# Performance work log

Hardware: AMD Instinct MI355X
Metric: run time of the kernel (lower is better)

## Reference

```python
import jax, jax.numpy as jnp
import numpy as np
import math
from jax import lax

B, T, GS = 16, 511, 1
OBS, OUT = 60, 30
D, H, L = 1024, 16, 8
DFF, HID = 4096, 100
S = T + GS
DH = D // H
EPS = 1e-5


def _ln(x, g, b):
    m = jnp.mean(x, axis=-1, keepdims=True)
    v = jnp.mean(jnp.square(x - m), axis=-1, keepdims=True)
    return (x - m) * lax.rsqrt(v + EPS) * g + b


def setup_inputs():
    key = jax.random.key(0)
    ks = iter(jax.random.split(key, 32))
    def n(shape):
        return jax.random.normal(next(ks), shape, dtype=jnp.float32) * 0.02
    return {
        "states": jax.random.normal(next(ks), (B, T, OBS), dtype=jnp.float32),
        "goals": jax.random.normal(next(ks), (B, GS, OBS), dtype=jnp.float32),
        "Wtok": n((OBS, D)), "btok": jnp.zeros((D,), jnp.float32),
        "pos": n((1, S, D)),
        "ln1_g": jnp.ones((L, D), jnp.float32), "ln1_b": jnp.zeros((L, D), jnp.float32),
        "Wq": n((L, D, D)), "bq": jnp.zeros((L, D), jnp.float32),
        "Wk": n((L, D, D)), "bk": jnp.zeros((L, D), jnp.float32),
        "Wv": n((L, D, D)), "bv": jnp.zeros((L, D), jnp.float32),
        "Wp": n((L, D, D)), "bp": jnp.zeros((L, D), jnp.float32),
        "ln2_g": jnp.ones((L, D), jnp.float32), "ln2_b": jnp.zeros((L, D), jnp.float32),
        "Wm1": n((L, D, DFF)), "bm1": jnp.zeros((L, DFF), jnp.float32),
        "Wm2": n((L, DFF, D)), "bm2": jnp.zeros((L, D), jnp.float32),
        "lnf_g": jnp.ones((D,), jnp.float32), "lnf_b": jnp.zeros((D,), jnp.float32),
        "Wh1": n((D, HID)), "bh1": jnp.zeros((HID,), jnp.float32),
        "Wh2": n((HID, OUT)), "bh2": jnp.zeros((OUT,), jnp.float32),
    }


def reference(states, goals, Wtok, btok, pos, ln1_g, ln1_b, Wq, bq, Wk, bk, Wv, bv, Wp, bp,
              ln2_g, ln2_b, Wm1, bm1, Wm2, bm2, lnf_g, lnf_b, Wh1, bh1, Wh2, bh2):
    # token + positional embeddings (dropout is identity in eval mode, pdrop=0)
    goal_x = goals @ Wtok + btok + pos[:, :GS]
    state_x = states @ Wtok + btok + pos[:, GS:S]
    x = jnp.concatenate([goal_x, state_x], axis=1)  # (B, S, D)
    mask = jnp.tril(jnp.ones((S, S), dtype=bool))
    scale = 1.0 / math.sqrt(DH)

    def block(x, p):
        g1, b1, wq, bq_, wk, bk_, wv, bv_, wp, bp_, g2, b2, w1, bm1_, w2, bm2_ = p
        h = _ln(x, g1, b1)
        q = (h @ wq + bq_).reshape(B, S, H, DH).transpose(0, 2, 1, 3)  # (B,H,S,DH)
        k = (h @ wk + bk_).reshape(B, S, H, DH).transpose(0, 2, 1, 3)
        v = (h @ wv + bv_).reshape(B, S, H, DH).transpose(0, 2, 1, 3)
        att = jnp.einsum('bhqd,bhkd->bhqk', q, k) * scale
        att = jnp.where(mask, att, -jnp.inf)
        att = jax.nn.softmax(att, axis=-1)
        y = jnp.einsum('bhqk,bhkd->bhqd', att, v)
        y = y.transpose(0, 2, 1, 3).reshape(B, S, D) @ wp + bp_
        x = x + y
        h = _ln(x, g2, b2)
        x = x + (jax.nn.gelu(h @ w1 + bm1_, approximate=False) @ w2 + bm2_)
        return x, None

    x, _ = lax.scan(block, x, (ln1_g, ln1_b, Wq, bq, Wk, bk, Wv, bv, Wp, bp,
                               ln2_g, ln2_b, Wm1, bm1, Wm2, bm2))
    x = _ln(x, lnf_g, lnf_b)[:, GS:]  # drop goal tokens -> (B, T, D)
    h = jax.nn.silu(x @ Wh1 + bh1)
    return h @ Wh2 + bh2
```

## Files before the change

kernel.cpp:

```cpp
#include <hip/hip_runtime.h>
#include <cstdint>
#include <math.h>

#define NB_B   16
#define NB_T   511
#define NB_S   512
#define NB_OBS 60
#define NB_D   1024
#define NB_H   16
#define NB_L   8
#define NB_DFF 4096
#define NB_HID 100
#define NB_OUT 30
#define NB_M   8192

typedef __attribute__((ext_vector_type(8))) short  short8;
typedef __attribute__((ext_vector_type(4))) short  short4v;
typedef __attribute__((ext_vector_type(4))) float  f32x4;
typedef __attribute__((ext_vector_type(8))) __bf16 bf16x8;

__device__ __forceinline__ short f2bf(float f) {
  union { float f; unsigned u; } a; a.f = f;
  unsigned u = a.u + 0x7fffu + ((a.u >> 16) & 1u);
  return (short)(u >> 16);
}

__device__ __forceinline__ void load_lds16(const void* g, void* l) {
  __builtin_amdgcn_global_load_lds(
      (__attribute__((address_space(1))) unsigned int*)(uintptr_t)g,
      (__attribute__((address_space(3))) unsigned int*)(unsigned)(uintptr_t)l,
      16, 0, 0);
}

__device__ __forceinline__ f32x4 mfma16(short8 a, short8 b, f32x4 c) {
  return __builtin_amdgcn_mfma_f32_16x16x32_bf16(
      __builtin_bit_cast(bf16x8, a), __builtin_bit_cast(bf16x8, b), c, 0, 0, 0);
}

__device__ __forceinline__ float gelu_exact(float v) {
  return 0.5f * v * (1.f + erff(v * 0.70710678118654752f));
}

__global__ __launch_bounds__(256) void tconv_kernel(
    const float* __restrict__ src, short* __restrict__ dst,
    int R, int C, size_t sstride, size_t dstride) {
  __shared__ float t[32][33];
  const float* s0 = src + blockIdx.z * sstride;
  short* d0 = dst + blockIdx.z * dstride;
  const int c0 = blockIdx.x * 32, r0 = blockIdx.y * 32;
  const int tx = threadIdx.x & 31, ty = threadIdx.x >> 5;
#pragma unroll
  for (int i = 0; i < 4; i++)
    t[ty + 8 * i][tx] = s0[(size_t)(r0 + ty + 8 * i) * C + c0 + tx];
  __syncthreads();
#pragma unroll
  for (int i = 0; i < 4; i++)
    d0[(size_t)(c0 + ty + 8 * i) * R + r0 + tx] = f2bf(t[tx][ty + 8 * i]);
}

__global__ __launch_bounds__(256) void whead_prep(
    const float* __restrict__ Wh1, const float* __restrict__ bh1,
    short* __restrict__ Wh1t, float* __restrict__ bh1p) {
  const int idx = blockIdx.x * 256 + threadIdx.x;
  const int n = idx >> 10, k = idx & 1023;
  Wh1t[idx] = (n < NB_HID) ? f2bf(Wh1[k * NB_HID + n]) : (short)0;
  if (idx < 128) bh1p[idx] = (idx < NB_HID) ? bh1[idx] : 0.f;
}

__global__ __launch_bounds__(256) void embed_kernel(
    const float* __restrict__ states, const float* __restrict__ goals,
    const float* __restrict__ Wtok, const float* __restrict__ btok,
    const float* __restrict__ pos, float* __restrict__ x) {
  const int row = blockIdx.x;
  const int b = row >> 9, s = row & (NB_S - 1);
  __shared__ float tok[NB_OBS];
  if (threadIdx.x < NB_OBS)
    tok[threadIdx.x] = (s == 0)
        ? goals[b * NB_OBS + threadIdx.x]
        : states[((size_t)b * NB_T + (s - 1)) * NB_OBS + threadIdx.x];
  __syncthreads();
#pragma unroll
  for (int i = 0; i < 4; i++) {
    const int d = threadIdx.x + i * 256;
    float acc = btok[d] + pos[(size_t)s * NB_D + d];
    for (int o = 0; o < NB_OBS; o++) acc += tok[o] * Wtok[o * NB_D + d];
    x[(size_t)row * NB_D + d] = acc;
  }
}

template <typename OutT>
__global__ __launch_bounds__(256) void ln_kernel(
    const float* __restrict__ xin, const float* __restrict__ gam,
    const float* __restrict__ bet, OutT* __restrict__ outp) {
  const int row = blockIdx.x;
  const int tid = threadIdx.x;
  const float4 v = ((const float4*)(xin + (size_t)row * NB_D))[tid];
  float s = v.x + v.y + v.z + v.w;
  float s2 = v.x * v.x + v.y * v.y + v.z * v.z + v.w * v.w;
#pragma unroll
  for (int o = 32; o; o >>= 1) {
    s += __shfl_down(s, o, 64);
    s2 += __shfl_down(s2, o, 64);
  }
  __shared__ float red[8];
  if ((tid & 63) == 0) { red[tid >> 6] = s; red[4 + (tid >> 6)] = s2; }
  __syncthreads();
  const float S1 = red[0] + red[1] + red[2] + red[3];
  const float S2 = red[4] + red[5] + red[6] + red[7];
  const float mean = S1 * (1.f / NB_D);
  const float var = S2 * (1.f / NB_D) - mean * mean;
  const float rs = rsqrtf(var + 1e-5f);
  const float4 g4 = ((const float4*)gam)[tid];
  const float4 b4 = ((const float4*)bet)[tid];
  const float o0 = (v.x - mean) * rs * g4.x + b4.x;
  const float o1 = (v.y - mean) * rs * g4.y + b4.y;
  const float o2 = (v.z - mean) * rs * g4.z + b4.z;
  const float o3 = (v.w - mean) * rs * g4.w + b4.w;
  if constexpr (sizeof(OutT) == 2) {
    short4v r = {f2bf(o0), f2bf(o1), f2bf(o2), f2bf(o3)};
    *(short4v*)((short*)outp + (size_t)row * NB_D + tid * 4) = r;
  } else {
    ((float4*)((float*)outp + (size_t)row * NB_D))[tid] = make_float4(o0, o1, o2, o3);
  }
}

template <int ACT, bool RESID, typename OutT>
__device__ __forceinline__ void gemm_core(
    const short* __restrict__ A, const short* __restrict__ Bt,
    const float* __restrict__ bias, const float* __restrict__ resid,
    OutT* __restrict__ C, int N, int K) {
  __shared__ short As[128][32];
  __shared__ short Bs[128][32];
  const int bm = blockIdx.y * 128, bn = blockIdx.x * 128;
  const int tid = threadIdx.x;
  const int w = tid >> 6, lane = tid & 63;
  const int wr = (w >> 1) * 64, wc = (w & 1) * 64;
  const int rr = lane & 15, sg = lane >> 4;

  f32x4 acc[4][4];
#pragma unroll
  for (int i = 0; i < 4; i++)
#pragma unroll
    for (int j = 0; j < 4; j++) acc[i][j] = f32x4{0.f, 0.f, 0.f, 0.f};

  const int srow0 = w * 32 + (lane >> 2);
  const int sslot = lane & 3;

  for (int k0 = 0; k0 < K; k0 += 32) {
    __syncthreads();
#pragma unroll
    for (int inst = 0; inst < 2; inst++) {
      const int r = srow0 + inst * 16;
      const int sl = sslot ^ ((r >> 1) & 3);
      load_lds16(A + (size_t)(bm + r) * K + k0 + sl * 8, &As[w * 32 + inst * 16][0]);
      load_lds16(Bt + (size_t)(bn + r) * K + k0 + sl * 8, &Bs[w * 32 + inst * 16][0]);
    }
    __syncthreads();
    short8 a[4], b[4];
#pragma unroll
    for (int i = 0; i < 4; i++) {
      const int r = wr + i * 16 + rr;
      a[i] = *(const short8*)&As[r][(sg ^ ((r >> 1) & 3)) * 8];
      const int c = wc + i * 16 + rr;
      b[i] = *(const short8*)&Bs[c][(sg ^ ((c >> 1) & 3)) * 8];
    }
#pragma unroll
    for (int i = 0; i < 4; i++)
#pragma unroll
      for (int j = 0; j < 4; j++) acc[i][j] = mfma16(a[i], b[j], acc[i][j]);
  }

#pragma unroll
  for (int j = 0; j < 4; j++) {
    const int col = bn + wc + j * 16 + rr;
    const float bv = bias[col];
#pragma unroll
    for (int i = 0; i < 4; i++) {
#pragma unroll
      for (int q = 0; q < 4; q++) {
        const int row = bm + wr + i * 16 + sg * 4 + q;
        float v = acc[i][j][q] + bv;
        if constexpr (RESID) v += resid[(size_t)row * N + col];
        if constexpr (ACT == 1) v = gelu_exact(v);
        if constexpr (ACT == 2) v = v / (1.f + __expf(-v));
        if constexpr (sizeof(OutT) == 2) C[(size_t)row * N + col] = (OutT)f2bf(v);
        else C[(size_t)row * N + col] = v;
      }
    }
  }
}

template <int ACT, bool RESID, typename OutT>
__global__ __launch_bounds__(256) void gemm_bt(
    const short* __restrict__ A, const short* __restrict__ Bt,
    const float* __restrict__ bias, const float* __restrict__ resid,
    OutT* __restrict__ C, int N, int K) {
  gemm_core<ACT, RESID, OutT>(A, Bt, bias, resid, C, N, K);
}

template <int ACT, bool RESID, typename OutT>
__device__ __forceinline__ void gemm8_core(
    const short* __restrict__ A, const short* __restrict__ Bt,
    const float* __restrict__ bias, const float* __restrict__ resid,
    OutT* __restrict__ C, int N, int K) {
  __shared__ short As[3][128][64];
  __shared__ short Bs[3][256][64];
  const int bm = blockIdx.y * 128, bn = blockIdx.x * 256;
  const int tid = threadIdx.x;
  const int w = tid >> 6, lane = tid & 63;
  const int wr = (w >> 2) * 64, wc = (w & 3) * 64;
  const int rr = lane & 15, sg = lane >> 4;
  const int lrow = lane >> 3;
  const int lslot = (lane & 7) ^ lrow;

  const short* Asrc = A + (size_t)(bm + w * 8 + lrow) * K + lslot * 8;
  const short* Bsrc = Bt + (size_t)(bn + w * 8 + lrow) * K + lslot * 8;

  auto stageA = [&](int buf, int c, int k0) {
    load_lds16(Asrc + (size_t)(c * 64) * K + k0, &As[buf][c * 64 + w * 8][0]);
  };
  auto stageB = [&](int buf, int c, int k0) {
    load_lds16(Bsrc + (size_t)(c * 64) * K + k0, &Bs[buf][c * 64 + w * 8][0]);
  };
  auto stage_tile = [&](int buf, int k0) {
    stageB(buf, 0, k0); stageB(buf, 1, k0); stageB(buf, 2, k0); stageB(buf, 3, k0);
    stageA(buf, 0, k0); stageA(buf, 1, k0);
  };

  f32x4 acc[4][4];
#pragma unroll
  for (int i = 0; i < 4; i++)
#pragma unroll
    for (int j = 0; j < 4; j++) acc[i][j] = f32x4{0.f, 0.f, 0.f, 0.f};

  const int nk = K >> 6;
  stage_tile(0, 0);
  stage_tile(1, 64);
  asm volatile("s_waitcnt vmcnt(6)" ::: "memory");
  asm volatile("s_barrier" ::: "memory");

  int bcur = 0, bnext = 1, bstage = 2;
  for (int t = 0; t < nk; ++t) {
    const bool do_stage = (t + 2 < nk);
    const int k2 = (t + 2) << 6;

    auto rdA = [&](int i, int kk) {
      const int r = wr + i * 16 + rr;
      return *(const short8*)&As[bcur][r][((kk * 4 + sg) ^ (r & 7)) * 8];
    };
    auto rdB = [&](int j, int kk) {
      const int r = wc + j * 16 + rr;
      return *(const short8*)&Bs[bcur][r][((kk * 4 + sg) ^ (r & 7)) * 8];
    };

    short8 a00 = rdA(0, 0), a01 = rdA(0, 1), a10 = rdA(1, 0), a11 = rdA(1, 1);
    short8 b00 = rdB(0, 0), b01 = rdB(0, 1), b10 = rdB(1, 0), b11 = rdB(1, 1);
    if (do_stage) { stageB(bstage, 0, k2); stageB(bstage, 1, k2); }
    asm volatile("s_barrier" ::: "memory");
    __builtin_amdgcn_s_setprio(1);
    acc[0][0] = mfma16(a00, b00, acc[0][0]); acc[0][0] = mfma16(a01, b01, acc[0][0]);
    acc[0][1] = mfma16(a00, b10, acc[0][1]); acc[0][1] = mfma16(a01, b11, acc[0][1]);
    acc[1][0] = mfma16(a10, b00, acc[1][0]); acc[1][0] = mfma16(a11, b01, acc[1][0]);
    acc[1][1] = mfma16(a10, b10, acc[1][1]); acc[1][1] = mfma16(a11, b11, acc[1][1]);
    __builtin_amdgcn_s_setprio(0);
    asm volatile("s_barrier" ::: "memory");

    short8 b20 = rdB(2, 0), b21 = rdB(2, 1), b30 = rdB(3, 0), b31 = rdB(3, 1);
    if (do_stage) { stageB(bstage, 2, k2); stageB(bstage, 3, k2); }
    asm volatile("s_barrier" ::: "memory");
    __builtin_amdgcn_s_setprio(1);
    acc[0][2] = mfma16(a00, b20, acc[0][2]); acc[0][2] = mfma16(a01, b21, acc[0][2]);
    acc[0][3] = mfma16(a00, b30, acc[0][3]); acc[0][3] = mfma16(a01, b31, acc[0][3]);
    acc[1][2] = mfma16(a10, b20, acc[1][2]); acc[1][2] = mfma16(a11, b21, acc[1][2]);
    acc[1][3] = mfma16(a10, b30, acc[1][3]); acc[1][3] = mfma16(a11, b31, acc[1][3]);
    __builtin_amdgcn_s_setprio(0);
    asm volatile("s_barrier" ::: "memory");

    short8 a20 = rdA(2, 0), a21 = rdA(2, 1), a30 = rdA(3, 0), a31 = rdA(3, 1);
    if (do_stage) { stageA(bstage, 0, k2); stageA(bstage, 1, k2); }
    asm volatile("s_barrier" ::: "memory");
    __builtin_amdgcn_s_setprio(1);
    acc[2][0] = mfma16(a20, b00, acc[2][0]); acc[2][0] = mfma16(a21, b01, acc[2][0]);
    acc[2][1] = mfma16(a20, b10, acc[2][1]); acc[2][1] = mfma16(a21, b11, acc[2][1]);
    acc[3][0] = mfma16(a30, b00, acc[3][0]); acc[3][0] = mfma16(a31, b01, acc[3][0]);
    acc[3][1] = mfma16(a30, b10, acc[3][1]); acc[3][1] = mfma16(a31, b11, acc[3][1]);
    __builtin_amdgcn_s_setprio(0);
    asm volatile("s_barrier" ::: "memory");

    if (do_stage)            asm volatile("s_waitcnt vmcnt(6)" ::: "memory");
    else if (t + 1 < nk)     asm volatile("s_waitcnt vmcnt(0)" ::: "memory");
    asm volatile("s_barrier" ::: "memory");
    __builtin_amdgcn_s_setprio(1);
    acc[2][2] = mfma16(a20, b20, acc[2][2]); acc[2][2] = mfma16(a21, b21, acc[2][2]);
    acc[2][3] = mfma16(a20, b30, acc[2][3]); acc[2][3] = mfma16(a21, b31, acc[2][3]);
    acc[3][2] = mfma16(a30, b20, acc[3][2]); acc[3][2] = mfma16(a31, b21, acc[3][2]);
    acc[3][3] = mfma16(a30, b30, acc[3][3]); acc[3][3] = mfma16(a31, b31, acc[3][3]);
    __builtin_amdgcn_s_setprio(0);
    asm volatile("s_barrier" ::: "memory");

    const int tmp = bcur; bcur = bnext; bnext = bstage; bstage = tmp;
  }

#pragma unroll
  for (int j = 0; j < 4; j++) {
    const int col = bn + wc + j * 16 + rr;
    const float bv = bias[col];
#pragma unroll
    for (int i = 0; i < 4; i++) {
#pragma unroll
      for (int q = 0; q < 4; q++) {
        const int row = bm + wr + i * 16 + sg * 4 + q;
        float v = acc[i][j][q] + bv;
        if constexpr (RESID) v += resid[(size_t)row * N + col];
        if constexpr (ACT == 1) v = gelu_exact(v);
        if constexpr (ACT == 2) v = v / (1.f + __expf(-v));
        if constexpr (sizeof(OutT) == 2) C[(size_t)row * N + col] = (OutT)f2bf(v);
        else C[(size_t)row * N + col] = v;
      }
    }
  }
}

template <int ACT, bool RESID, typename OutT>
__global__ __launch_bounds__(512) void gemm8_bt(
    const short* __restrict__ A, const short* __restrict__ Bt,
    const float* __restrict__ bias, const float* __restrict__ resid,
    OutT* __restrict__ C, int N, int K) {
  gemm8_core<ACT, RESID, OutT>(A, Bt, bias, resid, C, N, K);
}

__global__ __launch_bounds__(512) void gemm8_qkv_kernel(
    const short* __restrict__ A, const short* __restrict__ Wt3,
    const float* __restrict__ bq, const float* __restrict__ bk,
    const float* __restrict__ bv, short* __restrict__ outqkv) {
  const int z = blockIdx.z;
  const short* Bt = Wt3 + (size_t)z * NB_D * NB_D;
  const float* bias = (z == 0) ? bq : ((z == 1) ? bk : bv);
  short* C = outqkv + (size_t)z * NB_M * NB_D;
  gemm8_core<0, false, short>(A, Bt, bias, nullptr, C, NB_D, NB_D);
}

__global__ __launch_bounds__(256) void attn_kernel(
    const short* __restrict__ qkv, short* __restrict__ out) {
  const int qt = blockIdx.x, hh = blockIdx.y, bb = blockIdx.z;
  const int tid = threadIdx.x;
  const int w = tid >> 6, lane = tid & 63;
  const int rr = lane & 15, sg = lane >> 4;

  const size_t MD = (size_t)NB_M * NB_D;
  const short* Q = qkv;
  const short* K = qkv + MD;
  const short* V = qkv + 2 * MD;

  __shared__ short Ks[64][64];
  __shared__ short Vt[64][64];
  __shared__ short Ps[4][16][64];

  short8 qf[2];
  {
    const size_t qrow = (size_t)bb * NB_S + qt * 64 + w * 16 + rr;
#pragma unroll
    for (int ks = 0; ks < 2; ks++)
      qf[ks] = *(const short8*)&Q[qrow * NB_D + hh * 64 + ks * 32 + sg * 8];
  }

  float mrow[4], lrow[4];
  f32x4 o[4];
#pragma unroll
  for (int j = 0; j < 4; j++) { mrow[j] = -INFINITY; lrow[j] = 0.f; }
#pragma unroll
  for (int nb = 0; nb < 4; nb++) o[nb] = f32x4{0.f, 0.f, 0.f, 0.f};

  for (int kt = 0; kt <= qt; kt++) {
    __syncthreads();
    {
      const int p = lane & 7;
#pragma unroll
      for (int inst = 0; inst < 2; inst++) {
        const int r = w * 16 + inst * 8 + (lane >> 3);
        const int sl = p ^ (r & 7);
        load_lds16(K + ((size_t)bb * NB_S + kt * 64 + r) * NB_D + hh * 64 + sl * 8,
                   &Ks[w * 16 + inst * 8][0]);
      }
    }
    {
#pragma unroll
      for (int cc = 0; cc < 2; cc++) {
        const int c = tid * 2 + cc;
        const int sk = c >> 3, sl = c & 7;
        short8 vv = *(const short8*)&V[((size_t)bb * NB_S + kt * 64 + sk) * NB_D + hh * 64 + sl * 8];
        const int ss = sk >> 3;
#pragma unroll
        for (int j = 0; j < 8; j++) {
          const int dh = sl * 8 + j;
          Vt[dh][(ss ^ (dh & 7)) * 8 + (sk & 7)] = vv[j];
        }
      }
    }
    __syncthreads();

    f32x4 sf[4];
#pragma unroll
    for (int nb = 0; nb < 4; nb++) sf[nb] = f32x4{0.f, 0.f, 0.f, 0.f};
#pragma unroll
    for (int ks = 0; ks < 2; ks++) {
#pragma unroll
      for (int nb = 0; nb < 4; nb++) {
        const int ck = nb * 16 + rr;
        short8 kf = *(const short8*)&Ks[ck][((ks * 4 + sg) ^ (ck & 7)) * 8];
        sf[nb] = mfma16(qf[ks], kf, sf[nb]);
      }
    }
    const int rbase = qt * 64 + w * 16 + sg * 4;
    float pmax[4] = {-INFINITY, -INFINITY, -INFINITY, -INFINITY};
#pragma unroll
    for (int nb = 0; nb < 4; nb++) {
      const int cg = kt * 64 + nb * 16 + rr;
#pragma unroll
      for (int j = 0; j < 4; j++) {
        float sv = sf[nb][j] * 0.125f;
        if (cg > rbase + j) sv = -INFINITY;
        sf[nb][j] = sv;
        pmax[j] = fmaxf(pmax[j], sv);
      }
    }
#pragma unroll
    for (int o1 = 1; o1 < 16; o1 <<= 1)
#pragma unroll
      for (int j = 0; j < 4; j++)
        pmax[j] = fmaxf(pmax[j], __shfl_xor(pmax[j], o1, 64));

    float resc[4], psum[4];
#pragma unroll
    for (int j = 0; j < 4; j++) {
      const float mn = fmaxf(mrow[j], pmax[j]);
      resc[j] = __expf(mrow[j] - mn);
      mrow[j] = mn;
      psum[j] = 0.f;
    }
#pragma unroll
    for (int nb = 0; nb < 4; nb++)
#pragma unroll
      for (int j = 0; j < 4; j++) {
        const float p = __expf(sf[nb][j] - mrow[j]);
        sf[nb][j] = p;
        psum[j] += p;
      }
#pragma unroll
    for (int o1 = 1; o1 < 16; o1 <<= 1)
#pragma unroll
      for (int j = 0; j < 4; j++) psum[j] += __shfl_xor(psum[j], o1, 64);
#pragma unroll
    for (int j = 0; j < 4; j++) lrow[j] = lrow[j] * resc[j] + psum[j];
#pragma unroll
    for (int nb = 0; nb < 4; nb++)
#pragma unroll
      for (int j = 0; j < 4; j++) o[nb][j] *= resc[j];

#pragma unroll
    for (int nb = 0; nb < 4; nb++) {
      const int ck = nb * 16 + rr;
      const int ss = ck >> 3;
#pragma unroll
      for (int j = 0; j < 4; j++) {
        const int rq = sg * 4 + j;
        Ps[w][rq][(ss ^ (rq & 7)) * 8 + (ck & 7)] = f2bf(sf[nb][j]);
      }
    }
#pragma unroll
    for (int ks = 0; ks < 2; ks++) {
      short8 pf = *(const short8*)&Ps[w][rr][((ks * 4 + sg) ^ (rr & 7)) * 8];
#pragma unroll
      for (int nb = 0; nb < 4; nb++) {
        const int dh = nb * 16 + rr;
        short8 vf = *(const short8*)&Vt[dh][((ks * 4 + sg) ^ (dh & 7)) * 8];
        o[nb] = mfma16(pf, vf, o[nb]);
      }
    }
  }

  {
    const size_t orow0 = (size_t)bb * NB_S + qt * 64 + w * 16;
#pragma unroll
    for (int nb = 0; nb < 4; nb++)
#pragma unroll
      for (int j = 0; j < 4; j++) {
        const float v = o[nb][j] / lrow[j];
        out[(orow0 + sg * 4 + j) * NB_D + hh * 64 + nb * 16 + rr] = f2bf(v);
      }
  }
}

__global__ __launch_bounds__(256) void head2_kernel(
    const float* __restrict__ hbuf, const float* __restrict__ Wh2,
    const float* __restrict__ bh2, float* __restrict__ outp) {
  __shared__ float hs[8][NB_HID];
  const int g0 = blockIdx.x * 8;
  for (int idx = threadIdx.x; idx < 8 * NB_HID; idx += 256) {
    const int r = idx / NB_HID, k = idx - r * NB_HID;
    const int gt = g0 + r;
    const int b = gt / NB_T, tt = gt - b * NB_T;
    hs[r][k] = hbuf[(size_t)(b * NB_S + 1 + tt) * 128 + k];
  }
  __syncthreads();
  const int r = threadIdx.x >> 5, c = threadIdx.x & 31;
  if (c < NB_OUT) {
    float acc = bh2[c];
#pragma unroll
    for (int k = 0; k < NB_HID; k++) acc += hs[r][k] * Wh2[k * NB_OUT + c];
    outp[(size_t)(g0 + r) * NB_OUT + c] = acc;
  }
}

extern "C" void kernel_launch(void* const* d_in, const int* in_sizes, int n_in,
                              void* d_out, int out_size, void* d_ws, size_t ws_size,
                              hipStream_t stream) {
  const float* states = (const float*)d_in[0];
  const float* goals  = (const float*)d_in[1];
  const float* Wtok   = (const float*)d_in[2];
  const float* btok   = (const float*)d_in[3];
  const float* pos    = (const float*)d_in[4];
  const float* ln1_g  = (const float*)d_in[5];
  const float* ln1_b  = (const float*)d_in[6];
  const float* Wq     = (const float*)d_in[7];
  const float* bq     = (const float*)d_in[8];
  const float* Wk     = (const float*)d_in[9];
  const float* bk     = (const float*)d_in[10];
  const float* Wv     = (const float*)d_in[11];
  const float* bv     = (const float*)d_in[12];
  const float* Wp     = (const float*)d_in[13];
  const float* bp     = (const float*)d_in[14];
  const float* ln2_g  = (const float*)d_in[15];
  const float* ln2_b  = (const float*)d_in[16];
  const float* Wm1    = (const float*)d_in[17];
  const float* bm1    = (const float*)d_in[18];
  const float* Wm2    = (const float*)d_in[19];
  const float* bm2    = (const float*)d_in[20];
  const float* lnf_g  = (const float*)d_in[21];
  const float* lnf_b  = (const float*)d_in[22];
  const float* Wh1    = (const float*)d_in[23];
  const float* bh1    = (const float*)d_in[24];
  const float* Wh2    = (const float*)d_in[25];
  const float* bh2    = (const float*)d_in[26];

  char* wsp = (char*)d_ws;
  size_t off = 0;
  auto carve = [&](size_t bytes) -> char* {
    char* p = wsp + off;
    off += (bytes + 1023) & ~(size_t)1023;
    return p;
  };
  short* Wqkv_t = (short*)carve((size_t)NB_L * 3 * NB_D * NB_D * 2);
  short* Wp_t   = (short*)carve((size_t)NB_L * NB_D * NB_D * 2);
  short* Wm1_t  = (short*)carve((size_t)NB_L * NB_DFF * NB_D * 2);
  short* Wm2_t  = (short*)carve((size_t)NB_L * NB_D * NB_DFF * 2);
  float* x      = (float*)carve((size_t)NB_M * NB_D * 4);
  short* h      = (short*)carve((size_t)NB_M * NB_D * 2);
  short* qkvb   = (short*)carve((size_t)3 * NB_M * NB_D * 2);
  short* mlp    = (short*)carve((size_t)NB_M * NB_DFF * 2);
  short* Wh1t   = (short*)carve((size_t)128 * NB_D * 2);
  float* bh1p   = (float*)carve(128 * 4);
  short* attout = mlp;
  float* hbuf   = (float*)qkvb;

  const dim3 thr(256), thr8(512);
  const size_t DD = (size_t)NB_D * NB_D;
  const size_t DF = (size_t)NB_D * NB_DFF;

  tconv_kernel<<<dim3(32, 32, NB_L), thr, 0, stream>>>(Wq, Wqkv_t + 0 * DD, NB_D, NB_D, DD, 3 * DD);
  tconv_kernel<<<dim3(32, 32, NB_L), thr, 0, stream>>>(Wk, Wqkv_t + 1 * DD, NB_D, NB_D, DD, 3 * DD);
  tconv_kernel<<<dim3(32, 32, NB_L), thr, 0, stream>>>(Wv, Wqkv_t + 2 * DD, NB_D, NB_D, DD, 3 * DD);
  tconv_kernel<<<dim3(32, 32, NB_L), thr, 0, stream>>>(Wp, Wp_t, NB_D, NB_D, DD, DD);
  tconv_kernel<<<dim3(128, 32, NB_L), thr, 0, stream>>>(Wm1, Wm1_t, NB_D, NB_DFF, DF, DF);
  tconv_kernel<<<dim3(32, 128, NB_L), thr, 0, stream>>>(Wm2, Wm2_t, NB_DFF, NB_D, DF, DF);
  whead_prep<<<512, thr, 0, stream>>>(Wh1, bh1, Wh1t, bh1p);

  embed_kernel<<<NB_M, thr, 0, stream>>>(states, goals, Wtok, btok, pos, x);

  for (int l = 0; l < NB_L; l++) {
    ln_kernel<short><<<NB_M, thr, 0, stream>>>(x, ln1_g + l * NB_D, ln1_b + l * NB_D, h);
    gemm8_qkv_kernel<<<dim3(NB_D / 256, NB_M / 128, 3), thr8, 0, stream>>>(
        h, Wqkv_t + (size_t)l * 3 * DD, bq + l * NB_D, bk + l * NB_D, bv + l * NB_D, qkvb);
    attn_kernel<<<dim3(NB_S / 64, NB_H, NB_B), thr, 0, stream>>>(qkvb, attout);
    gemm8_bt<0, true, float><<<dim3(NB_D / 256, NB_M / 128), thr8, 0, stream>>>(
        attout, Wp_t + (size_t)l * DD, bp + l * NB_D, x, x, NB_D, NB_D);
    ln_kernel<short><<<NB_M, thr, 0, stream>>>(x, ln2_g + l * NB_D, ln2_b + l * NB_D, h);
    gemm8_bt<1, false, short><<<dim3(NB_DFF / 256, NB_M / 128), thr8, 0, stream>>>(
        h, Wm1_t + (size_t)l * DF, bm1 + l * NB_DFF, nullptr, mlp, NB_DFF, NB_D);
    gemm8_bt<0, true, float><<<dim3(NB_D / 256, NB_M / 128), thr8, 0, stream>>>(
        mlp, Wm2_t + (size_t)l * DF, bm2 + l * NB_D, x, x, NB_D, NB_DFF);
  }

  ln_kernel<short><<<NB_M, thr, 0, stream>>>(x, lnf_g, lnf_b, h);
  gemm_bt<2, false, float><<<dim3(1, NB_M / 128), thr, 0, stream>>>(
      h, Wh1t, bh1p, nullptr, hbuf, 128, NB_D);
  head2_kernel<<<NB_M / 8, thr, 0, stream>>>(hbuf, Wh2, bh2, (float*)d_out);
}
```

Before: 3.385 ms.

## Restructure bf16 GEMM main loop with compile-time K, unrolled buffers, and tile swizzle

Makes K a template parameter and unrolls the triple-buffered k-loop by three so buffer indices become compile-time constants with precomputed LDS offsets. Each k-tile drops from four MFMA phases with paired barriers to two larger phases that read all B fragments up front. It also remaps workgroup IDs so groups of eight consecutive blocks cover strided output tiles for better L2 reuse, and vectorises the epilogue bias and residual handling. The fewer barriers and larger phases raise register pressure, and the block remap changes cache behaviour.

```diff
diff --git a/kernel.cpp b/kernel.cpp
--- a/kernel.cpp
+++ b/kernel.cpp
@@ -18,6 +18,8 @@
 typedef __attribute__((ext_vector_type(4))) short  short4v;
 typedef __attribute__((ext_vector_type(4))) float  f32x4;
 typedef __attribute__((ext_vector_type(8))) __bf16 bf16x8;
+
+template <int N_> struct ic { static constexpr int v = N_; };
 
 __device__ __forceinline__ short f2bf(float f) {
   union { float f; unsigned u; } a; a.f = f;
@@ -125,7 +127,7 @@
 }
 
 template <int ACT, bool RESID, typename OutT>
-__device__ __forceinline__ void gemm_core(
+__global__ __launch_bounds__(256) void gemm_bt(
     const short* __restrict__ A, const short* __restrict__ Bt,
     const float* __restrict__ bias, const float* __restrict__ resid,
     OutT* __restrict__ C, int N, int K) {
@@ -190,22 +192,23 @@
   }
 }
 
-template <int ACT, bool RESID, typename OutT>
-__global__ __launch_bounds__(256) void gemm_bt(
-    const short* __restrict__ A, const short* __restrict__ Bt,
-    const float* __restrict__ bias, const float* __restrict__ resid,
-    OutT* __restrict__ C, int N, int K) {
-  gemm_core<ACT, RESID, OutT>(A, Bt, bias, resid, C, N, K);
-}
-
-template <int ACT, bool RESID, typename OutT>
+template <int K, int ACT, bool RESID, typename OutT>
 __device__ __forceinline__ void gemm8_core(
     const short* __restrict__ A, const short* __restrict__ Bt,
     const float* __restrict__ bias, const float* __restrict__ resid,
-    OutT* __restrict__ C, int N, int K) {
-  __shared__ short As[3][128][64];
-  __shared__ short Bs[3][256][64];
-  const int bm = blockIdx.y * 128, bn = blockIdx.x * 256;
+    OutT* __restrict__ C, int N) {
+  constexpr int NK = K / 64;
+  __shared__ short As[3][128 * 64];
+  __shared__ short Bs[3][256 * 64];
+
+  const int gx = N >> 8;
+  int wg = blockIdx.x + gx * blockIdx.y;
+  {
+    const int q = (gx * (NB_M / 128)) >> 3;
+    wg = (wg & 7) * q + (wg >> 3);
+  }
+  const int bm = (wg / gx) * 128, bn = (wg % gx) * 256;
+
   const int tid = threadIdx.x;
   const int w = tid >> 6, lane = tid & 63;
   const int wr = (w >> 2) * 64, wc = (w & 3) * 64;
@@ -215,118 +218,165 @@
 
   const short* Asrc = A + (size_t)(bm + w * 8 + lrow) * K + lslot * 8;
   const short* Bsrc = Bt + (size_t)(bn + w * 8 + lrow) * K + lslot * 8;
-
-  auto stageA = [&](int buf, int c, int k0) {
-    load_lds16(Asrc + (size_t)(c * 64) * K + k0, &As[buf][c * 64 + w * 8][0]);
+  short* Adst = &As[0][(w * 8) * 64];
+  short* Bdst = &Bs[0][(w * 8) * 64];
+
+  const int ar = wr + rr, br = wc + rr;
+  const int aoff0 = ar * 64 + ((0 + sg) ^ (ar & 7)) * 8;
+  const int aoff1 = ar * 64 + ((4 + sg) ^ (ar & 7)) * 8;
+  const int boff0 = br * 64 + ((0 + sg) ^ (br & 7)) * 8;
+  const int boff1 = br * 64 + ((4 + sg) ^ (br & 7)) * 8;
+
+  f32x4 acc[4][4];
+#pragma unroll
+  for (int i = 0; i < 4; i++)
+#pragma unroll
+    for (int j = 0; j < 4; j++) acc[i][j] = f32x4{0.f, 0.f, 0.f, 0.f};
+
+  auto stage_tile = [&](int sb, int k0) {
+    load_lds16(Bsrc + k0,                      Bdst + sb * 16384);
+    load_lds16(Bsrc + (size_t)64 * K + k0,     Bdst + sb * 16384 + 4096);
+    load_lds16(Bsrc + (size_t)128 * K + k0,    Bdst + sb * 16384 + 8192);
+    load_lds16(Bsrc + (size_t)192 * K + k0,    Bdst + sb * 16384 + 12288);
+    load_lds16(Asrc + k0,                      Adst + sb * 8192);
+    load_lds16(Asrc + (size_t)64 * K + k0,     Adst + sb * 8192 + 4096);
   };
-  auto stageB = [&](int buf, int c, int k0) {
-    load_lds16(Bsrc + (size_t)(c * 64) * K + k0, &Bs[buf][c * 64 + w * 8][0]);
-  };
-  auto stage_tile = [&](int buf, int k0) {
-    stageB(buf, 0, k0); stageB(buf, 1, k0); stageB(buf, 2, k0); stageB(buf, 3, k0);
-    stageA(buf, 0, k0); stageA(buf, 1, k0);
-  };
-
-  f32x4 acc[4][4];
-#pragma unroll
-  for (int i = 0; i < 4; i++)
-#pragma unroll
-    for (int j = 0; j < 4; j++) acc[i][j] = f32x4{0.f, 0.f, 0.f, 0.f};
-
-  const int nk = K >> 6;
+
   stage_tile(0, 0);
   stage_tile(1, 64);
   asm volatile("s_waitcnt vmcnt(6)" ::: "memory");
-  asm volatile("s_barrier" ::: "memory");
-
-  int bcur = 0, bnext = 1, bstage = 2;
-  for (int t = 0; t < nk; ++t) {
-    const bool do_stage = (t + 2 < nk);
-    const int k2 = (t + 2) << 6;
-
-    auto rdA = [&](int i, int kk) {
-      const int r = wr + i * 16 + rr;
-      return *(const short8*)&As[bcur][r][((kk * 4 + sg) ^ (r & 7)) * 8];
-    };
-    auto rdB = [&](int j, int kk) {
-      const int r = wc + j * 16 + rr;
-      return *(const short8*)&Bs[bcur][r][((kk * 4 + sg) ^ (r & 7)) * 8];
-    };
-
-    short8 a00 = rdA(0, 0), a01 = rdA(0, 1), a10 = rdA(1, 0), a11 = rdA(1, 1);
-    short8 b00 = rdB(0, 0), b01 = rdB(0, 1), b10 = rdB(1, 0), b11 = rdB(1, 1);
-    if (do_stage) { stageB(bstage, 0, k2); stageB(bstage, 1, k2); }
-    asm volatile("s_barrier" ::: "memory");
+  __builtin_amdgcn_s_barrier();
+
+  auto ktile = [&](auto BUFC, auto SBUFC, int t) {
+    constexpr int BUF = decltype(BUFC)::v;
+    constexpr int SBUF = decltype(SBUFC)::v;
+    const bool ds = (t + 2 < NK);
+    const int k2 = (t + 2) * 64;
+    const short* Ab = As[BUF];
+    const short* Bb = Bs[BUF];
+
+    short8 a00 = *(const short8*)(Ab + aoff0);
+    short8 a01 = *(const short8*)(Ab + aoff1);
+    short8 a10 = *(const short8*)(Ab + aoff0 + 1024);
+    short8 a11 = *(const short8*)(Ab + aoff1 + 1024);
+    short8 b00 = *(const short8*)(Bb + boff0);
+    short8 b01 = *(const short8*)(Bb + boff1);
+    short8 b10 = *(const short8*)(Bb + boff0 + 1024);
+    short8 b11 = *(const short8*)(Bb + boff1 + 1024);
+    short8 b20 = *(const short8*)(Bb + boff0 + 2048);
+    short8 b21 = *(const short8*)(Bb + boff1 + 2048);
+    short8 b30 = *(const short8*)(Bb + boff0 + 3072);
+    short8 b31 = *(const short8*)(Bb + boff1 + 3072);
+    if (ds) {
+      load_lds16(Bsrc + k2,                   Bdst + SBUF * 16384);
+      load_lds16(Bsrc + (size_t)64 * K + k2,  Bdst + SBUF * 16384 + 4096);
+      load_lds16(Bsrc + (size_t)128 * K + k2, Bdst + SBUF * 16384 + 8192);
+      load_lds16(Bsrc + (size_t)192 * K + k2, Bdst + SBUF * 16384 + 12288);
+    }
+    __builtin_amdgcn_s_barrier();
+    asm volatile("s_waitcnt lgkmcnt(0)" ::: "memory");
     __builtin_amdgcn_s_setprio(1);
-    acc[0][0] = mfma16(a00, b00, acc[0][0]); acc[0][0] = mfma16(a01, b01, acc[0][0]);
-    acc[0][1] = mfma16(a00, b10, acc[0][1]); acc[0][1] = mfma16(a01, b11, acc[0][1]);
-    acc[1][0] = mfma16(a10, b00, acc[1][0]); acc[1][0] = mfma16(a11, b01, acc[1][0]);
-    acc[1][1] = mfma16(a10, b10, acc[1][1]); acc[1][1] = mfma16(a11, b11, acc[1][1]);
+    acc[0][0] = mfma16(a00, b00, acc[0][0]);
+    acc[0][1] = mfma16(a00, b10, acc[0][1]);
+    acc[0][2] = mfma16(a00, b20, acc[0][2]);
+    acc[0][3] = mfma16(a00, b30, acc[0][3]);
+    acc[1][0] = mfma16(a10, b00, acc[1][0]);
+    acc[1][1] = mfma16(a10, b10, acc[1][1]);
+    acc[1][2] = mfma16(a10, b20, acc[1][2]);
+    acc[1][3] = mfma16(a10, b30, acc[1][3]);
+    acc[0][0] = mfma16(a01, b01, acc[0][0]);
+    acc[0][1] = mfma16(a01, b11, acc[0][1]);
+    acc[0][2] = mfma16(a01, b21, acc[0][2]);
+    acc[0][3] = mfma16(a01, b31, acc[0][3]);
+    acc[1][0] = mfma16(a11, b01, acc[1][0]);
+    acc[1][1] = mfma16(a11, b11, acc[1][1]);
+    acc[1][2] = mfma16(a11, b21, acc[1][2]);
+    acc[1][3] = mfma16(a11, b31, acc[1][3]);
     __builtin_amdgcn_s_setprio(0);
-    asm volatile("s_barrier" ::: "memory");
-
-    short8 b20 = rdB(2, 0), b21 = rdB(2, 1), b30 = rdB(3, 0), b31 = rdB(3, 1);
-    if (do_stage) { stageB(bstage, 2, k2); stageB(bstage, 3, k2); }
-    asm volatile("s_barrier" ::: "memory");
+    __builtin_amdgcn_s_barrier();
+
+    short8 a20 = *(const short8*)(Ab + aoff0 + 2048);
+    short8 a21 = *(const short8*)(Ab + aoff1 + 2048);
+    short8 a30 = *(const short8*)(Ab + aoff0 + 3072);
+    short8 a31 = *(const short8*)(Ab + aoff1 + 3072);
+    if (ds) {
+      load_lds16(Asrc + k2,                  Adst + SBUF * 8192);
+      load_lds16(Asrc + (size_t)64 * K + k2, Adst + SBUF * 8192 + 4096);
+    }
+    __builtin_amdgcn_s_barrier();
+    asm volatile("s_waitcnt lgkmcnt(0)" ::: "memory");
     __builtin_amdgcn_s_setprio(1);
-    acc[0][2] = mfma16(a00, b20, acc[0][2]); acc[0][2] = mfma16(a01, b21, acc[0][2]);
-    acc[0][3] = mfma16(a00, b30, acc[0][3]); acc[0][3] = mfma16(a01, b31, acc[0][3]);
-    acc[1][2] = mfma16(a10, b20, acc[1][2]); acc[1][2] = mfma16(a11, b21, acc[1][2]);
-    acc[1][3] = mfma16(a10, b30, acc[1][3]); acc[1][3] = mfma16(a11, b31, acc[1][3]);
+    acc[2][0] = mfma16(a20, b00, acc[2][0]);
+    acc[2][1] = mfma16(a20, b10, acc[2][1]);
+    acc[2][2] = mfma16(a20, b20, acc[2][2]);
+    acc[2][3] = mfma16(a20, b30, acc[2][3]);
+    acc[3][0] = mfma16(a30, b00, acc[3][0]);
+    acc[3][1] = mfma16(a30, b10, acc[3][1]);
+    acc[3][2] = mfma16(a30, b20, acc[3][2]);
+    acc[3][3] = mfma16(a30, b30, acc[3][3]);
+    acc[2][0] = mfma16(a21, b01, acc[2][0]);
+    acc[2][1] = mfma16(a21, b11, acc[2][1]);
+    acc[2][2] = mfma16(a21, b21, acc[2][2]);
+    acc[2][3] = mfma16(a21, b31, acc[2][3]);
+    acc[3][0] = mfma16(a31, b01, acc[3][0]);
+    acc[3][1] = mfma16(a31, b11, acc[3][1]);
+    acc[3][2] = mfma16(a31, b21, acc[3][2]);
+    acc[3][3] = mfma16(a31, b31, acc[3][3]);
     __builtin_amdgcn_s_setprio(0);
-    asm volatile("s_barrier" ::: "memory");
-
-    short8 a20 = rdA(2, 0), a21 = rdA(2, 1), a30 = rdA(3, 0), a31 = rdA(3, 1);
-    if (do_stage) { stageA(bstage, 0, k2); stageA(bstage, 1, k2); }
-    asm volatile("s_barrier" ::: "memory");
-    __builtin_amdgcn_s_setprio(1);
-    acc[2][0] = mfma16(a20, b00, acc[2][0]); acc[2][0] = mfma16(a21, b01, acc[2][0]);
-    acc[2][1] = mfma16(a20, b10, acc[2][1]); acc[2][1] = mfma16(a21, b11, acc[2][1]);
-    acc[3][0] = mfma16(a30, b00, acc[3][0]); acc[3][0] = mfma16(a31, b01, acc[3][0]);
-    acc[3][1] = mfma16(a30, b10, acc[3][1]); acc[3][1] = mfma16(a31, b11, acc[3][1]);
-    __builtin_amdgcn_s_setprio(0);
-    asm volatile("s_barrier" ::: "memory");
-
-    if (do_stage)            asm volatile("s_waitcnt vmcnt(6)" ::: "memory");
-    else if (t + 1 < nk)     asm volatile("s_waitcnt vmcnt(0)" ::: "memory");
-    asm volatile("s_barrier" ::: "memory");
-    __builtin_amdgcn_s_setprio(1);
-    acc[2][2] = mfma16(a20, b20, acc[2][2]); acc[2][2] = mfma16(a21, b21, acc[2][2]);
-    acc[2][3] = mfma16(a20, b30, acc[2][3]); acc[2][3] = mfma16(a21, b31, acc[2][3]);
-    acc[3][2] = mfma16(a30, b20, acc[3][2]); acc[3][2] = mfma16(a31, b21, acc[3][2]);
-    acc[3][3] = mfma16(a30, b30, acc[3][3]); acc[3][3] = mfma16(a31, b31, acc[3][3]);
-    __builtin_amdgcn_s_setprio(0);
-    asm volatile("s_barrier" ::: "memory");
-
-    const int tmp = bcur; bcur = bnext; bnext = bstage; bstage = tmp;
-  }
-
-#pragma unroll
-  for (int j = 0; j < 4; j++) {
-    const int col = bn + wc + j * 16 + rr;
-    const float bv = bias[col];
-#pragma unroll
-    for (int i = 0; i < 4; i++) {
-#pragma unroll
-      for (int q = 0; q < 4; q++) {
-        const int row = bm + wr + i * 16 + sg * 4 + q;
-        float v = acc[i][j][q] + bv;
-        if constexpr (RESID) v += resid[(size_t)row * N + col];
-        if constexpr (ACT == 1) v = gelu_exact(v);
-        if constexpr (ACT == 2) v = v / (1.f + __expf(-v));
-        if constexpr (sizeof(OutT) == 2) C[(size_t)row * N + col] = (OutT)f2bf(v);
-        else C[(size_t)row * N + col] = v;
-      }
-    }
-  }
-}
-
-template <int ACT, bool RESID, typename OutT>
-__global__ __launch_bounds__(512) void gemm8_bt(
+    if (ds)              asm volatile("s_waitcnt vmcnt(6)" ::: "memory");
+    else if (t + 1 < NK) asm volatile("s_waitcnt vmcnt(0)" ::: "memory");
+    __builtin_amdgcn_s_barrier();
+  };
+
+  int t = 0;
+#pragma unroll 1
+  for (; t + 3 <= NK; t += 3) {
+    ktile(ic<0>{}, ic<2>{}, t);
+    ktile(ic<1>{}, ic<0>{}, t + 1);
+    ktile(ic<2>{}, ic<1>{}, t + 2);
+  }
+  if constexpr (NK % 3 >= 1) ktile(ic<0>{}, ic<2>{}, NK - NK % 3);
+  if constexpr (NK % 3 >= 2) ktile(ic<1>{}, ic<0>{}, NK - NK % 3 + 1);
+
+  const int col0 = bn + wc + rr;
+  const float bv0 = bias[col0];
+  const float bv1 = bias[col0 + 16];
+  const float bv2 = bias[col0 + 32];
+  const float bv3 = bias[col0 + 48];
+#pragma unroll
+  for (int i = 0; i < 4; i++) {
+#pragma unroll
+    for (int q = 0; q < 4; q++) {
+      const size_t row = bm + wr + i * 16 + sg * 4 + q;
+      float v0 = acc[i][0][q] + bv0;
+      float v1 = acc[i][1][q] + bv1;
+      float v2 = acc[i][2][q] + bv2;
+      float v3 = acc[i][3][q] + bv3;
+      if constexpr (RESID) {
+        const float* rrow = resid + row * N + col0;
+        v0 += rrow[0]; v1 += rrow[16]; v2 += rrow[32]; v3 += rrow[48];
+      }
+      if constexpr (ACT == 1) {
+        v0 = gelu_exact(v0); v1 = gelu_exact(v1);
+        v2 = gelu_exact(v2); v3 = gelu_exact(v3);
+      }
+      OutT* crow = C + row * N + col0;
+      if constexpr (sizeof(OutT) == 2) {
+        crow[0] = (OutT)f2bf(v0); crow[16] = (OutT)f2bf(v1);
+        crow[32] = (OutT)f2bf(v2); crow[48] = (OutT)f2bf(v3);
+      } else {
+        crow[0] = v0; crow[16] = v1; crow[32] = v2; crow[48] = v3;
+      }
+    }
+  }
+}
+
+template <int K, int ACT, bool RESID, typename OutT>
+__global__ __launch_bounds__(512) void gemm8(
     const short* __restrict__ A, const short* __restrict__ Bt,
     const float* __restrict__ bias, const float* __restrict__ resid,
-    OutT* __restrict__ C, int N, int K) {
-  gemm8_core<ACT, RESID, OutT>(A, Bt, bias, resid, C, N, K);
+    OutT* __restrict__ C, int N) {
+  gemm8_core<K, ACT, RESID, OutT>(A, Bt, bias, resid, C, N);
 }
 
 __global__ __launch_bounds__(512) void gemm8_qkv_kernel(
@@ -337,7 +387,7 @@
   const short* Bt = Wt3 + (size_t)z * NB_D * NB_D;
   const float* bias = (z == 0) ? bq : ((z == 1) ? bk : bv);
   short* C = outqkv + (size_t)z * NB_M * NB_D;
-  gemm8_core<0, false, short>(A, Bt, bias, nullptr, C, NB_D, NB_D);
+  gemm8_core<NB_D, 0, false, short>(A, Bt, bias, nullptr, C, NB_D);
 }
 
 __global__ __launch_bounds__(256) void attn_kernel(
@@ -582,13 +632,13 @@
     gemm8_qkv_kernel<<<dim3(NB_D / 256, NB_M / 128, 3), thr8, 0, stream>>>(
         h, Wqkv_t + (size_t)l * 3 * DD, bq + l * NB_D, bk + l * NB_D, bv + l * NB_D, qkvb);
     attn_kernel<<<dim3(NB_S / 64, NB_H, NB_B), thr, 0, stream>>>(qkvb, attout);
-    gemm8_bt<0, true, float><<<dim3(NB_D / 256, NB_M / 128), thr8, 0, stream>>>(
-        attout, Wp_t + (size_t)l * DD, bp + l * NB_D, x, x, NB_D, NB_D);
+    gemm8<NB_D, 0, true, float><<<dim3(NB_D / 256, NB_M / 128), thr8, 0, stream>>>(
+        attout, Wp_t + (size_t)l * DD, bp + l * NB_D, x, x, NB_D);
     ln_kernel<short><<<NB_M, thr, 0, stream>>>(x, ln2_g + l * NB_D, ln2_b + l * NB_D, h);
-    gemm8_bt<1, false, short><<<dim3(NB_DFF / 256, NB_M / 128), thr8, 0, stream>>>(
-        h, Wm1_t + (size_t)l * DF, bm1 + l * NB_DFF, nullptr, mlp, NB_DFF, NB_D);
-    gemm8_bt<0, true, float><<<dim3(NB_D / 256, NB_M / 128), thr8, 0, stream>>>(
-        mlp, Wm2_t + (size_t)l * DF, bm2 + l * NB_D, x, x, NB_D, NB_DFF);
+    gemm8<NB_D, 1, false, short><<<dim3(NB_DFF / 256, NB_M / 128), thr8, 0, stream>>>(
+        h, Wm1_t + (size_t)l * DF, bm1 + l * NB_DFF, nullptr, mlp, NB_DFF);
+    gemm8<NB_DFF, 0, true, float><<<dim3(NB_D / 256, NB_M / 128), thr8, 0, stream>>>(
+        mlp, Wm2_t + (size_t)l * DF, bm2 + l * NB_D, x, x, NB_D);
   }
 
   ln_kernel<short><<<NB_M, thr, 0, stream>>>(x, lnf_g, lnf_b, h);
```

After: 3.157 ms. 1.07x faster.
